# Kernel tuning notes

Hardware: AMD Instinct MI355X
Metric: run time of the kernel (lower is better)

The kernel has to match this reference:

```python
import jax, jax.numpy as jnp
import numpy as np
from jax import lax

DN = ('NHWC', 'HWIO', 'NHWC')
EPS = 1e-7


def squash(s, axis=-1):
    sq = jnp.sum(s * s, axis=axis, keepdims=True)
    return s * (sq / (1.0 + sq) / jnp.sqrt(sq + EPS))


def setup_inputs() -> dict:
    key = jax.random.key(0)
    ks = jax.random.split(key, 4)
    inputs = jax.random.normal(ks[0], (2, 250, 250, 3), dtype=jnp.float32)
    conv_w = jax.random.normal(ks[1], (9, 9, 3, 256), dtype=jnp.float32) * 0.02
    conv_b = jnp.zeros((256,), dtype=jnp.float32)
    pc_w = jax.random.normal(ks[2], (9, 9, 256, 128), dtype=jnp.float32) * 0.02
    pc_b = jnp.zeros((128,), dtype=jnp.float32)
    # CapsLayer routing weights: [num_caps=8, in_caps=219024, dim_caps=8, in_dim=8]
    W_caps = jax.random.normal(ks[3], (8, 219024, 8, 8), dtype=jnp.float32) * 0.05
    return {"inputs": inputs, "conv_w": conv_w, "conv_b": conv_b,
            "pc_w": pc_w, "pc_b": pc_b, "W_caps": W_caps}


def reference(inputs, conv_w, conv_b, pc_w, pc_b, W_caps):
    ROUTINGS = 3
    B = inputs.shape[0]
    # Conv backbone: 250x250x3 -> 242x242x256, ReLU
    x = lax.conv_general_dilated(inputs, conv_w, (1, 1), 'VALID', dimension_numbers=DN)
    x = jax.nn.relu(x + conv_b)
    # PrimaryCaps: linear conv (128 ch, k=9, s=2, valid) -> 117x117x128 -> [B, 219024, 8] -> squash
    pc = lax.conv_general_dilated(x, pc_w, (2, 2), 'VALID', dimension_numbers=DN) + pc_b
    u = squash(pc.reshape(B, -1, 8))  # [B, N=219024, 8]
    # Prediction vectors u_hat[b,j,i,o] = W[j,i,o,d] u[b,i,d]
    u_hat = jnp.einsum('jiod,bid->bjio', W_caps, u)  # [B, J, N, 8]
    J, N = W_caps.shape[0], W_caps.shape[1]
    b_logits = jnp.zeros((B, J, N), dtype=u_hat.dtype)
    v = None
    for r in range(ROUTINGS):
        c = jax.nn.softmax(b_logits, axis=1)          # coupling over output caps
        s = jnp.einsum('bji,bjio->bjo', c, u_hat)     # [B, J, 8]
        v = squash(s)
        if r < ROUTINGS - 1:
            b_logits = b_logits + jnp.einsum('bjo,bjio->bji', v, u_hat)
    return v  # [B, 8, 8]
```

## Files before the change

### kernel.cpp

```cpp
#include <hip/hip_runtime.h>

#define N_CAPS 219024
#define J_CAPS 8

typedef __attribute__((ext_vector_type(8))) __bf16 bf16x8;
typedef __attribute__((ext_vector_type(4))) float  f32x4;
typedef __attribute__((ext_vector_type(8))) short  short8;

typedef const __attribute__((address_space(1))) unsigned int gld_t;
typedef __attribute__((address_space(3))) unsigned int lds_t;

__device__ __forceinline__ unsigned short f2bf(float f) {
    unsigned int u = __float_as_uint(f);
    u = (u + 0x7FFFu + ((u >> 16) & 1u)) >> 16;
    return (unsigned short)u;
}

__global__ __launch_bounds__(256) void conv1_kernel(
    const float* __restrict__ in, const float* __restrict__ w,
    const float* __restrict__ bias, unsigned short* __restrict__ out)
{
    const int oc  = threadIdx.x;
    const int ox0 = blockIdx.x * 16;
    const int oy  = blockIdx.y;
    const int b   = blockIdx.z;

    __shared__ float lin[9][24][3];
    for (int idx = threadIdx.x; idx < 9 * 24 * 3; idx += 256) {
        int r   = idx / (24 * 3);
        int rem = idx - r * (24 * 3);
        int col = rem / 3;
        int c   = rem - col * 3;
        int iy  = oy + r;
        int ix  = ox0 + col;
        float v = 0.f;
        if (ix < 250) v = in[((b * 250 + iy) * 250 + ix) * 3 + c];
        lin[r][col][c] = v;
    }
    __syncthreads();

    float acc[16];
#pragma unroll
    for (int t = 0; t < 16; ++t) acc[t] = 0.f;

    for (int ky = 0; ky < 9; ++ky) {
#pragma unroll
        for (int ic = 0; ic < 3; ++ic) {
            float xv[24];
#pragma unroll
            for (int c2 = 0; c2 < 24; ++c2) xv[c2] = lin[ky][c2][ic];
#pragma unroll
            for (int kx = 0; kx < 9; ++kx) {
                float wv = w[((ky * 9 + kx) * 3 + ic) * 256 + oc];
#pragma unroll
                for (int t = 0; t < 16; ++t)
                    acc[t] += xv[kx + t] * wv;
            }
        }
    }

    float bv = bias[oc];
#pragma unroll
    for (int t = 0; t < 16; ++t) {
        int ox = ox0 + t;
        if (ox < 242) {
            float v = acc[t] + bv;
            out[((b * 242 + oy) * 242 + ox) * 256 + oc] = f2bf(v > 0.f ? v : 0.f);
        }
    }
}

__global__ __launch_bounds__(256) void w2_convert_kernel(
    const float* __restrict__ w, unsigned short* __restrict__ wt)
{
    int idx = blockIdx.x * 256 + threadIdx.x;
    if (idx >= 81 * 128 * 256) return;
    int ic = idx & 255;
    int t  = idx >> 8;
    int oc = t & 127;
    int p  = t >> 7;
    wt[idx] = f2bf(w[(p * 256 + ic) * 128 + oc]);
}

__global__ __launch_bounds__(256, 4) void conv2_mfma_kernel(
    const unsigned short* __restrict__ x1bf,
    const unsigned short* __restrict__ w2t,
    const float* __restrict__ bias,
    float* __restrict__ out)
{
    const int bx   = blockIdx.x;
    const int oy   = blockIdx.y;
    const int b    = blockIdx.z;
    const int tid  = threadIdx.x;
    const int wave = tid >> 6;
    const int lane = tid & 63;
    const int li   = lane & 15;
    const int quad = lane >> 4;
    const int wn   = wave * 32;
    const int ox0  = bx * 64;

    __shared__ __align__(16) unsigned short As[2][135 * 64];

    f32x4 acc[4][2];
#pragma unroll
    for (int mt = 0; mt < 4; ++mt) {
        acc[mt][0] = (f32x4){0.f, 0.f, 0.f, 0.f};
        acc[mt][1] = (f32x4){0.f, 0.f, 0.f, 0.f};
    }

    const int n0 = wn + li;
    const int n1 = wn + 16 + li;
    const size_t bofs0 = (size_t)n0 * 256 + quad * 8;
    const size_t bofs1 = (size_t)n1 * 256 + quad * 8;

    const unsigned short* xbase =
        x1bf + ((size_t)(b * 242 + 2 * oy) * 242 + 2 * ox0) * 256;

    auto stage = [&](int p) {
        const int ky = p >> 2;
        const int q  = p & 3;
        const unsigned short* xr = xbase + (size_t)ky * (242 * 256) + q * 64;
        unsigned short* db = &As[p & 1][0];
#pragma unroll
        for (int it = 0; it < 5; ++it) {
            int ct = it * 256 + tid;
            if (ct < 135 * 8) {
                int col = ct >> 3;
                int cc  = ct & 7;
                int src = cc ^ ((col >> 1) & 7);
                __builtin_amdgcn_global_load_lds(
                    (gld_t*)(xr + (size_t)col * 256 + src * 8),
                    (lds_t*)(db + (size_t)(it * 256 + wave * 64) * 8),
                    16, 0, 0);
            }
        }
    };

    stage(0);
    __syncthreads();

    for (int p = 0; p < 36; ++p) {
        if (p < 35) stage(p + 1);

        const int ky = p >> 2;
        const int q  = p & 3;
        const unsigned short* asb = As[p & 1];

        for (int kx = 0; kx < 9; ++kx) {
            const unsigned short* wp =
                w2t + ((size_t)(ky * 9 + kx) << 15) + q * 64;
            const int sw = (li + (kx >> 1)) & 7;
            const int colb = 2 * li + kx;
#pragma unroll
            for (int kc = 0; kc < 2; ++kc) {
                bf16x8 b0 = *(const bf16x8*)&wp[bofs0 + kc * 32];
                bf16x8 b1 = *(const bf16x8*)&wp[bofs1 + kc * 32];
                const int c4 = ((kc << 2) + quad) ^ sw;
#pragma unroll
                for (int mt = 0; mt < 4; ++mt) {
                    bf16x8 a = *(const bf16x8*)&asb[(size_t)(mt * 32 + colb) * 64 + c4 * 8];
                    acc[mt][0] = __builtin_amdgcn_mfma_f32_16x16x32_bf16(a, b0, acc[mt][0], 0, 0, 0);
                    acc[mt][1] = __builtin_amdgcn_mfma_f32_16x16x32_bf16(a, b1, acc[mt][1], 0, 0, 0);
                }
            }
        }
        __syncthreads();
    }

    const float bv0 = bias[n0];
    const float bv1 = bias[n1];
#pragma unroll
    for (int mt = 0; mt < 4; ++mt) {
#pragma unroll
        for (int r = 0; r < 4; ++r) {
            const int m  = mt * 16 + quad * 4 + r;
            const int ox = ox0 + m;
            if (ox < 117) {
                float* op = &out[((size_t)(b * 117 + oy) * 117 + ox) * 128];
                op[n0] = acc[mt][0][r] + bv0;
                op[n1] = acc[mt][1][r] + bv1;
            }
        }
    }
}

__global__ __launch_bounds__(256) void squash_u_kernel(float* data, int n_groups)
{
    int i = blockIdx.x * 256 + threadIdx.x;
    if (i >= n_groups) return;
    float4* p = (float4*)(data + (size_t)i * 8);
    float4 a = p[0], c = p[1];
    float sq = a.x * a.x + a.y * a.y + a.z * a.z + a.w * a.w
             + c.x * c.x + c.y * c.y + c.z * c.z + c.w * c.w;
    float scale = (sq / (1.f + sq)) * rsqrtf(sq + 1e-7f);
    p[0] = make_float4(a.x * scale, a.y * scale, a.z * scale, a.w * scale);
    p[1] = make_float4(c.x * scale, c.y * scale, c.z * scale, c.w * scale);
}

__global__ __launch_bounds__(256) void uhat_kernel(
    const float* __restrict__ W, const float* __restrict__ u,
    float* __restrict__ uhat)
{
    int idx = blockIdx.x * 256 + threadIdx.x;
    if (idx >= J_CAPS * N_CAPS) return;
    int j = idx / N_CAPS;
    int i = idx - j * N_CAPS;

    const float4* wp = (const float4*)(W + (size_t)idx * 64);
    const float4* u0 = (const float4*)(u + (size_t)i * 8);
    const float4* u1 = (const float4*)(u + ((size_t)N_CAPS + i) * 8);
    float4 u0a = u0[0], u0b = u0[1];
    float4 u1a = u1[0], u1b = u1[1];

    float o0[8], o1[8];
#pragma unroll
    for (int o = 0; o < 8; ++o) {
        float4 wa = wp[2 * o], wb = wp[2 * o + 1];
        o0[o] = wa.x * u0a.x + wa.y * u0a.y + wa.z * u0a.z + wa.w * u0a.w
              + wb.x * u0b.x + wb.y * u0b.y + wb.z * u0b.z + wb.w * u0b.w;
        o1[o] = wa.x * u1a.x + wa.y * u1a.y + wa.z * u1a.z + wa.w * u1a.w
              + wb.x * u1b.x + wb.y * u1b.y + wb.z * u1b.z + wb.w * u1b.w;
    }
    float4* d0 = (float4*)(uhat + ((size_t)(0 * J_CAPS + j) * N_CAPS + i) * 8);
    float4* d1 = (float4*)(uhat + ((size_t)(1 * J_CAPS + j) * N_CAPS + i) * 8);
    d0[0] = make_float4(o0[0], o0[1], o0[2], o0[3]);
    d0[1] = make_float4(o0[4], o0[5], o0[6], o0[7]);
    d1[0] = make_float4(o1[0], o1[1], o1[2], o1[3]);
    d1[1] = make_float4(o1[4], o1[5], o1[6], o1[7]);
}

template <int MODE>
__global__ __launch_bounds__(256) void routing_kernel(
    const float* __restrict__ uhat, const float* __restrict__ vprev,
    const float* __restrict__ b_in, float* __restrict__ b_out,
    float* __restrict__ s)
{
    const int bb = blockIdx.y;
    __shared__ float vsh[64];
    __shared__ float ssh[64];
    if (threadIdx.x < 64) {
        ssh[threadIdx.x] = 0.f;
        vsh[threadIdx.x] = (MODE > 0) ? vprev[bb * 64 + threadIdx.x] : 0.f;
    }
    __syncthreads();

    float acc[64];
#pragma unroll
    for (int k = 0; k < 64; ++k) acc[k] = 0.f;

    const float* ub = uhat + (size_t)bb * J_CAPS * (size_t)N_CAPS * 8;
    for (int i = blockIdx.x * 256 + threadIdx.x; i < N_CAPS; i += gridDim.x * 256) {
        float uh[64];
#pragma unroll
        for (int j = 0; j < 8; ++j) {
            const float* p = ub + ((size_t)j * N_CAPS + i) * 8;
            float4 x0 = *(const float4*)p;
            float4 x1 = *(const float4*)(p + 4);
            uh[j * 8 + 0] = x0.x; uh[j * 8 + 1] = x0.y;
            uh[j * 8 + 2] = x0.z; uh[j * 8 + 3] = x0.w;
            uh[j * 8 + 4] = x1.x; uh[j * 8 + 5] = x1.y;
            uh[j * 8 + 6] = x1.z; uh[j * 8 + 7] = x1.w;
        }
        float c[8];
        if (MODE == 0) {
#pragma unroll
            for (int j = 0; j < 8; ++j) c[j] = 0.125f;
        } else {
            float bj[8];
#pragma unroll
            for (int j = 0; j < 8; ++j) {
                float d = 0.f;
#pragma unroll
                for (int o = 0; o < 8; ++o) d += vsh[j * 8 + o] * uh[j * 8 + o];
                bj[j] = d;
            }
            if (MODE == 2) {
#pragma unroll
                for (int j = 0; j < 8; ++j)
                    bj[j] += b_in[((size_t)bb * 8 + j) * N_CAPS + i];
            } else {
#pragma unroll
                for (int j = 0; j < 8; ++j)
                    b_out[((size_t)bb * 8 + j) * N_CAPS + i] = bj[j];
            }
            float m = bj[0];
#pragma unroll
            for (int j = 1; j < 8; ++j) m = fmaxf(m, bj[j]);
            float se = 0.f;
#pragma unroll
            for (int j = 0; j < 8; ++j) { c[j] = __expf(bj[j] - m); se += c[j]; }
            float inv = 1.f / se;
#pragma unroll
            for (int j = 0; j < 8; ++j) c[j] *= inv;
        }
#pragma unroll
        for (int k = 0; k < 64; ++k) acc[k] += c[k >> 3] * uh[k];
    }

#pragma unroll
    for (int k = 0; k < 64; ++k) {
        float v = acc[k];
        for (int off = 32; off > 0; off >>= 1)
            v += __shfl_down(v, off, 64);
        if ((threadIdx.x & 63) == 0) atomicAdd(&ssh[k], v);
    }
    __syncthreads();
    if (threadIdx.x < 64) atomicAdd(&s[bb * 64 + threadIdx.x], ssh[threadIdx.x]);
}

__global__ void squash_v_kernel(const float* __restrict__ s, float* __restrict__ v)
{
    int t = threadIdx.x;
    if (t >= 16) return;
    const float4* p = (const float4*)(s + t * 8);
    float4 a = p[0], c = p[1];
    float sq = a.x * a.x + a.y * a.y + a.z * a.z + a.w * a.w
             + c.x * c.x + c.y * c.y + c.z * c.z + c.w * c.w;
    float scale = (sq / (1.f + sq)) * rsqrtf(sq + 1e-7f);
    float4* d = (float4*)(v + t * 8);
    d[0] = make_float4(a.x * scale, a.y * scale, a.z * scale, a.w * scale);
    d[1] = make_float4(c.x * scale, c.y * scale, c.z * scale, c.w * scale);
}

__global__ void zero_kernel(float* p, int n)
{
    int i = blockIdx.x * 256 + threadIdx.x;
    if (i < n) p[i] = 0.f;
}

extern "C" void kernel_launch(void* const* d_in, const int* in_sizes, int n_in,
                              void* d_out, int out_size, void* d_ws, size_t ws_size,
                              hipStream_t stream)
{
    const float* in = (const float*)d_in[0];
    const float* w1 = (const float*)d_in[1];
    const float* b1 = (const float*)d_in[2];
    const float* w2 = (const float*)d_in[3];
    const float* b2 = (const float*)d_in[4];
    const float* Wc = (const float*)d_in[5];
    float* out = (float*)d_out;
    char* wsb  = (char*)d_ws;

    float*          uhat = (float*)wsb;
    unsigned short* x1bf = (unsigned short*)wsb;
    float*          pc   = (float*)(wsb + 112140288);
    float*          blog = (float*)(wsb + 126157824);
    unsigned short* w2t  = (unsigned short*)(wsb + 140175360);
    float*          sbuf = (float*)(wsb + 145483776);
    float*          vbuf = (float*)(wsb + 145484288);

    w2_convert_kernel<<<(81 * 128 * 256 + 255) / 256, 256, 0, stream>>>(w2, w2t);
    conv1_kernel<<<dim3(16, 242, 2), 256, 0, stream>>>(in, w1, b1, x1bf);
    conv2_mfma_kernel<<<dim3(2, 117, 2), 256, 0, stream>>>(x1bf, w2t, b2, pc);
    squash_u_kernel<<<(2 * N_CAPS + 255) / 256, 256, 0, stream>>>(pc, 2 * N_CAPS);
    uhat_kernel<<<(J_CAPS * N_CAPS + 255) / 256, 256, 0, stream>>>(Wc, pc, uhat);

    zero_kernel<<<1, 128, 0, stream>>>(sbuf, 128);
    routing_kernel<0><<<dim3(256, 2), 256, 0, stream>>>(uhat, nullptr, nullptr, nullptr, sbuf);
    squash_v_kernel<<<1, 64, 0, stream>>>(sbuf, vbuf);

    zero_kernel<<<1, 128, 0, stream>>>(sbuf, 128);
    routing_kernel<1><<<dim3(256, 2), 256, 0, stream>>>(uhat, vbuf, nullptr, blog, sbuf);
    squash_v_kernel<<<1, 64, 0, stream>>>(sbuf, vbuf);

    zero_kernel<<<1, 128, 0, stream>>>(sbuf, 128);
    routing_kernel<2><<<dim3(256, 2), 256, 0, stream>>>(uhat, vbuf, blog, nullptr, sbuf);
    squash_v_kernel<<<1, 64, 0, stream>>>(sbuf, out);
}
```

Measured before the change: 1.271 ms.

## Split conv2 reduction over kernel rows into three partials, fuse sum into squash

The PrimaryCaps conv is split along the ky dimension into three independent blocks per output tile, tripling the grid from 468 to 1404 blocks so more CUs are busy. Each block writes fp32 partial sums to a workspace buffer, and the squash kernel now sums the three partials, adds the bias and applies squash in one pass. The LDS tile is padded (528-element row groups) to reduce bank conflicts, and conv1's shared tile is transposed to channel-major so the per-channel reads are contiguous. The cost is the extra traffic of writing and reading three partial output tensors.

```diff
diff --git a/kernel.cpp b/kernel.cpp
--- a/kernel.cpp
+++ b/kernel.cpp
@@ -25,7 +25,7 @@
     const int oy  = blockIdx.y;
     const int b   = blockIdx.z;
 
-    __shared__ float lin[9][24][3];
+    __shared__ float lin[9][3][24];
     for (int idx = threadIdx.x; idx < 9 * 24 * 3; idx += 256) {
         int r   = idx / (24 * 3);
         int rem = idx - r * (24 * 3);
@@ -35,7 +35,7 @@
         int ix  = ox0 + col;
         float v = 0.f;
         if (ix < 250) v = in[((b * 250 + iy) * 250 + ix) * 3 + c];
-        lin[r][col][c] = v;
+        lin[r][c][col] = v;
     }
     __syncthreads();
 
@@ -48,7 +48,7 @@
         for (int ic = 0; ic < 3; ++ic) {
             float xv[24];
 #pragma unroll
-            for (int c2 = 0; c2 < 24; ++c2) xv[c2] = lin[ky][c2][ic];
+            for (int c2 = 0; c2 < 24; ++c2) xv[c2] = lin[ky][ic][c2];
 #pragma unroll
             for (int kx = 0; kx < 9; ++kx) {
                 float wv = w[((ky * 9 + kx) * 3 + ic) * 256 + oc];
@@ -85,12 +85,13 @@
 __global__ __launch_bounds__(256, 4) void conv2_mfma_kernel(
     const unsigned short* __restrict__ x1bf,
     const unsigned short* __restrict__ w2t,
-    const float* __restrict__ bias,
-    float* __restrict__ out)
+    float* __restrict__ part)
 {
     const int bx   = blockIdx.x;
     const int oy   = blockIdx.y;
-    const int b    = blockIdx.z;
+    const int bz   = blockIdx.z;
+    const int b    = bz & 1;
+    const int kys  = bz >> 1;
     const int tid  = threadIdx.x;
     const int wave = tid >> 6;
     const int lane = tid & 63;
@@ -98,8 +99,9 @@
     const int quad = lane >> 4;
     const int wn   = wave * 32;
     const int ox0  = bx * 64;
-
-    __shared__ __align__(16) unsigned short As[2][135 * 64];
+    const int ky0  = kys * 3;
+
+    __shared__ __align__(16) unsigned short As[2][8976];
 
     f32x4 acc[4][2];
 #pragma unroll
@@ -117,7 +119,7 @@
         x1bf + ((size_t)(b * 242 + 2 * oy) * 242 + 2 * ox0) * 256;
 
     auto stage = [&](int p) {
-        const int ky = p >> 2;
+        const int ky = ky0 + (p >> 2);
         const int q  = p & 3;
         const unsigned short* xr = xbase + (size_t)ky * (242 * 256) + q * 64;
         unsigned short* db = &As[p & 1][0];
@@ -130,7 +132,7 @@
                 int src = cc ^ ((col >> 1) & 7);
                 __builtin_amdgcn_global_load_lds(
                     (gld_t*)(xr + (size_t)col * 256 + src * 8),
-                    (lds_t*)(db + (size_t)(it * 256 + wave * 64) * 8),
+                    (lds_t*)(db + (size_t)(ct >> 6) * 528 + (size_t)(ct & 63) * 8),
                     16, 0, 0);
             }
         }
@@ -139,18 +141,19 @@
     stage(0);
     __syncthreads();
 
-    for (int p = 0; p < 36; ++p) {
-        if (p < 35) stage(p + 1);
-
-        const int ky = p >> 2;
+    for (int p = 0; p < 12; ++p) {
+        if (p < 11) stage(p + 1);
+
+        const int ky = ky0 + (p >> 2);
         const int q  = p & 3;
         const unsigned short* asb = As[p & 1];
 
         for (int kx = 0; kx < 9; ++kx) {
             const unsigned short* wp =
                 w2t + ((size_t)(ky * 9 + kx) << 15) + q * 64;
-            const int sw = (li + (kx >> 1)) & 7;
-            const int colb = 2 * li + kx;
+            const int colb0 = 2 * li + kx;
+            const int base0 = (colb0 >> 3) * 528 + (colb0 & 7) * 64;
+            const int sw    = (colb0 >> 1) & 7;
 #pragma unroll
             for (int kc = 0; kc < 2; ++kc) {
                 bf16x8 b0 = *(const bf16x8*)&wp[bofs0 + kc * 32];
@@ -158,7 +161,7 @@
                 const int c4 = ((kc << 2) + quad) ^ sw;
 #pragma unroll
                 for (int mt = 0; mt < 4; ++mt) {
-                    bf16x8 a = *(const bf16x8*)&asb[(size_t)(mt * 32 + colb) * 64 + c4 * 8];
+                    bf16x8 a = *(const bf16x8*)&asb[base0 + mt * 2112 + c4 * 8];
                     acc[mt][0] = __builtin_amdgcn_mfma_f32_16x16x32_bf16(a, b0, acc[mt][0], 0, 0, 0);
                     acc[mt][1] = __builtin_amdgcn_mfma_f32_16x16x32_bf16(a, b1, acc[mt][1], 0, 0, 0);
                 }
@@ -167,8 +170,8 @@
         __syncthreads();
     }
 
-    const float bv0 = bias[n0];
-    const float bv1 = bias[n1];
+    float* pp = part + (size_t)kys * (2ull * 117 * 117 * 128)
+              + (size_t)(b * 117 + oy) * 117 * 128;
 #pragma unroll
     for (int mt = 0; mt < 4; ++mt) {
 #pragma unroll
@@ -176,25 +179,45 @@
             const int m  = mt * 16 + quad * 4 + r;
             const int ox = ox0 + m;
             if (ox < 117) {
-                float* op = &out[((size_t)(b * 117 + oy) * 117 + ox) * 128];
-                op[n0] = acc[mt][0][r] + bv0;
-                op[n1] = acc[mt][1][r] + bv1;
-            }
-        }
-    }
-}
-
-__global__ __launch_bounds__(256) void squash_u_kernel(float* data, int n_groups)
-{
-    int i = blockIdx.x * 256 + threadIdx.x;
-    if (i >= n_groups) return;
-    float4* p = (float4*)(data + (size_t)i * 8);
-    float4 a = p[0], c = p[1];
-    float sq = a.x * a.x + a.y * a.y + a.z * a.z + a.w * a.w
-             + c.x * c.x + c.y * c.y + c.z * c.z + c.w * c.w;
+                float* op = pp + (size_t)ox * 128;
+                op[n0] = acc[mt][0][r];
+                op[n1] = acc[mt][1][r];
+            }
+        }
+    }
+}
+
+__global__ __launch_bounds__(256) void squash_u_kernel(
+    const float* __restrict__ part, const float* __restrict__ bias,
+    float* __restrict__ u, int n_groups)
+{
+    int g = blockIdx.x * 256 + threadIdx.x;
+    if (g >= n_groups) return;
+    const size_t PSZ = 2ull * 117 * 117 * 128;
+    const float4* p0 = (const float4*)(part + (size_t)g * 8);
+    const float4* p1 = (const float4*)(part + PSZ + (size_t)g * 8);
+    const float4* p2 = (const float4*)(part + 2 * PSZ + (size_t)g * 8);
+    const float4* bp = (const float4*)(bias + (g & 15) * 8);
+    float4 a0 = p0[0], c0 = p0[1];
+    float4 a1 = p1[0], c1 = p1[1];
+    float4 a2 = p2[0], c2 = p2[1];
+    float4 ba = bp[0], bc = bp[1];
+    float x[8];
+    x[0] = a0.x + a1.x + a2.x + ba.x;
+    x[1] = a0.y + a1.y + a2.y + ba.y;
+    x[2] = a0.z + a1.z + a2.z + ba.z;
+    x[3] = a0.w + a1.w + a2.w + ba.w;
+    x[4] = c0.x + c1.x + c2.x + bc.x;
+    x[5] = c0.y + c1.y + c2.y + bc.y;
+    x[6] = c0.z + c1.z + c2.z + bc.z;
+    x[7] = c0.w + c1.w + c2.w + bc.w;
+    float sq = 0.f;
+#pragma unroll
+    for (int j = 0; j < 8; ++j) sq += x[j] * x[j];
     float scale = (sq / (1.f + sq)) * rsqrtf(sq + 1e-7f);
-    p[0] = make_float4(a.x * scale, a.y * scale, a.z * scale, a.w * scale);
-    p[1] = make_float4(c.x * scale, c.y * scale, c.z * scale, c.w * scale);
+    float4* d = (float4*)(u + (size_t)g * 8);
+    d[0] = make_float4(x[0] * scale, x[1] * scale, x[2] * scale, x[3] * scale);
+    d[1] = make_float4(x[4] * scale, x[5] * scale, x[6] * scale, x[7] * scale);
 }
 
 __global__ __launch_bounds__(256) void uhat_kernel(
@@ -341,18 +364,19 @@
     float* out = (float*)d_out;
     char* wsb  = (char*)d_ws;
 
-    float*          uhat = (float*)wsb;
-    unsigned short* x1bf = (unsigned short*)wsb;
-    float*          pc   = (float*)(wsb + 112140288);
-    float*          blog = (float*)(wsb + 126157824);
-    unsigned short* w2t  = (unsigned short*)(wsb + 140175360);
-    float*          sbuf = (float*)(wsb + 145483776);
-    float*          vbuf = (float*)(wsb + 145484288);
+    float*          uhat   = (float*)wsb;
+    unsigned short* x1bf   = (unsigned short*)wsb;
+    float*          pcpart = (float*)(wsb + 59969536);
+    float*          pc     = (float*)(wsb + 112140288);
+    float*          blog   = (float*)(wsb + 126157824);
+    unsigned short* w2t    = (unsigned short*)(wsb + 140175360);
+    float*          sbuf   = (float*)(wsb + 145483776);
+    float*          vbuf   = (float*)(wsb + 145484288);
 
     w2_convert_kernel<<<(81 * 128 * 256 + 255) / 256, 256, 0, stream>>>(w2, w2t);
     conv1_kernel<<<dim3(16, 242, 2), 256, 0, stream>>>(in, w1, b1, x1bf);
-    conv2_mfma_kernel<<<dim3(2, 117, 2), 256, 0, stream>>>(x1bf, w2t, b2, pc);
-    squash_u_kernel<<<(2 * N_CAPS + 255) / 256, 256, 0, stream>>>(pc, 2 * N_CAPS);
+    conv2_mfma_kernel<<<dim3(2, 117, 6), 256, 0, stream>>>(x1bf, w2t, pcpart);
+    squash_u_kernel<<<(2 * N_CAPS + 255) / 256, 256, 0, stream>>>(pcpart, b2, pc, 2 * N_CAPS);
     uhat_kernel<<<(J_CAPS * N_CAPS + 255) / 256, 256, 0, stream>>>(Wc, pc, uhat);
 
     zero_kernel<<<1, 128, 0, stream>>>(sbuf, 128);
```

Result: no change. 1.258 ms (-1.0%).
